# Performance work log

Measured on AMD Instinct MI355X. Metric: run time of the kernel, lower is better.

The kernel has to match this reference:

```python
import jax, jax.numpy as jnp
import numpy as np

H = 4        # attention heads
C = 32       # embedding_size (out_channels per head)
B = 8        # graphs per batch
NPER = 2048  # nodes (Hi-C bins) per graph
N = B * NPER
E = 1048576  # edges (avg degree 64)
IN = 4       # input_embedding_size
ED = 1       # edge_dim
EPS = 1e-5


def setup_inputs() -> dict:
    key = jax.random.key(0)
    ks = jax.random.split(key, 20)
    x = jax.random.normal(ks[0], (N, IN), jnp.float32)
    # edges stay within their graph so the per-graph reshape in
    # process_graph_batch is semantically consistent
    g = jax.random.randint(ks[1], (E,), 0, B)
    src = g * NPER + jax.random.randint(ks[2], (E,), 0, NPER)
    dst = g * NPER + jax.random.randint(ks[3], (E,), 0, NPER)
    edge_index = jnp.stack([src, dst]).astype(jnp.int32)
    edge_attr = jax.random.uniform(ks[4], (E, ED), jnp.float32)
    batch_index = jnp.repeat(jnp.arange(B, dtype=jnp.int32), NPER)

    def lin(k, i, o):
        return jax.random.normal(k, (i, o), jnp.float32) / np.float32(np.sqrt(i))

    HC = H * C
    inp = dict(
        x=x, edge_index=edge_index, edge_attr=edge_attr, batch_index=batch_index,
        Wq=lin(ks[5], IN, HC), bq=jnp.zeros((HC,), jnp.float32),
        Wk=lin(ks[6], IN, HC), bk=jnp.zeros((HC,), jnp.float32),
        Wv=lin(ks[7], IN, HC), bv=jnp.zeros((HC,), jnp.float32),
        We=lin(ks[8], ED, HC), be=jnp.zeros((HC,), jnp.float32),
        Ws=lin(ks[9], IN, HC), bs=jnp.zeros((HC,), jnp.float32),
        Wbeta=lin(ks[10], 3 * HC, 1),
        Wl=lin(ks[11], HC, C), bl=jnp.zeros((C,), jnp.float32),
        gn_w=jnp.ones((C,), jnp.float32),
        gn_b=jnp.zeros((C,), jnp.float32),
        gn_ms=jnp.ones((C,), jnp.float32),
    )
    return inp


def reference(x, edge_index, edge_attr, batch_index,
              Wq, bq, Wk, bk, Wv, bv, We, be, Ws, bs, Wbeta,
              Wl, bl, gn_w, gn_b, gn_ms):
    src, dst = edge_index[0], edge_index[1]
    n = x.shape[0]
    e = src.shape[0]

    # ---- TransformerConv(in=4, out=32, heads=4, edge_dim=1, beta=True) ----
    q = (x @ Wq + bq).reshape(n, H, C)
    k = (x @ Wk + bk).reshape(n, H, C)
    v = (x @ Wv + bv).reshape(n, H, C)
    ee = (edge_attr @ We + be).reshape(e, H, C)

    kj = k[src] + ee               # [E,H,C] key of source + edge embedding
    vj = v[src] + ee               # [E,H,C]
    qi = q[dst]                    # [E,H,C]
    alpha = jnp.sum(qi * kj, axis=-1) / jnp.sqrt(jnp.float32(C))  # [E,H]

    # segment softmax over incoming edges of each destination node
    amax = jax.ops.segment_max(alpha, dst, num_segments=n)        # [N,H]
    amax = jnp.where(jnp.isfinite(amax), amax, 0.0)
    alpha = jnp.exp(alpha - jax.lax.stop_gradient(amax)[dst])
    denom = jax.ops.segment_sum(alpha, dst, num_segments=n)       # [N,H]
    denom = jnp.where(denom > 0, denom, 1.0)
    alpha = alpha / denom[dst]

    out = jax.ops.segment_sum(alpha[..., None] * vj, dst, num_segments=n)
    out = out.reshape(n, H * C)    # concat heads

    # beta skip connection (root_weight + gated residual)
    x_r = x @ Ws + bs              # [N,H*C]
    beta = jax.nn.sigmoid(jnp.concatenate([out, x_r, out - x_r], axis=-1) @ Wbeta)
    out = beta * x_r + (1.0 - beta) * out

    # ---- Linear + relu ----
    h = jax.nn.relu(out @ Wl + bl)  # [N,C]

    # ---- GraphNorm over each graph in the batch ----
    ones = jnp.ones((n, 1), h.dtype)
    cnt = jax.ops.segment_sum(ones, batch_index, num_segments=B)        # [B,1]
    mean = jax.ops.segment_sum(h, batch_index, num_segments=B) / cnt    # [B,C]
    hc = h - gn_ms * mean[batch_index]
    var = jax.ops.segment_sum(hc * hc, batch_index, num_segments=B) / cnt
    h = hc / jnp.sqrt(var[batch_index] + EPS) * gn_w + gn_b

    # ---- process_graph_batch + InnerProductDecoder ----
    Z = h.reshape(B, NPER, C)
    adj = jax.nn.sigmoid(jnp.einsum('bnc,bmc->bnm', Z, Z))
    return adj[:, None, :, :]      # [B,1,NPER,NPER]
```

## Files before the change

### kernel.cpp

```cpp
#include <hip/hip_runtime.h>

#define NGRAPH 8
#define NPER 2048
#define NN 16384
#define EE 1048576
#define BSH 5
#define NB (NN >> BSH)
#define NPB (1 << BSH)
#define SEG 4096
#define CAP 3584
#define SBLK 128
#define EPB (EE/SBLK)
#define XBOUND 8.0f
#define RSQRT_C 0.17677669529663687f

typedef __attribute__((ext_vector_type(8))) short short8v;
typedef __attribute__((ext_vector_type(4))) float f32x4;

__device__ __forceinline__ float sigmoidf_(float v){ return 1.0f/(1.0f + __expf(-v)); }

__device__ __forceinline__ unsigned short f2bf(float v){
  unsigned u = __float_as_uint(v);
  unsigned r = (u + 0x7FFFu + ((u >> 16) & 1u)) >> 16;
  return (unsigned short)r;
}
__device__ __forceinline__ float bf2f(unsigned short h){
  return __uint_as_float(((unsigned)h) << 16);
}

__global__ __launch_bounds__(256) void k_pre(const float* __restrict__ x,
                      const float* __restrict__ Wq, const float* __restrict__ bq,
                      const float* __restrict__ Wk, const float* __restrict__ bk,
                      const float* __restrict__ be, const float* __restrict__ We,
                      unsigned* __restrict__ cursor,
                      float* __restrict__ P){
  if (blockIdx.x < 2){
    const int b = blockIdx.x*256 + threadIdx.x;
    cursor[b] = (unsigned)b * SEG;
  }
  const int tid = blockIdx.x*256 + threadIdx.x;
  const int n = tid >> 2, h = tid & 3;
  const float4 xn = *(const float4*)&x[n*4];
  float a0=0.f,a1=0.f,a2=0.f,a3=0.f,qw=0.f,bb=0.f;
#pragma unroll
  for (int c=0;c<32;c++){
    int hc = h*32 + c;
    float q = bq[hc] + xn.x*Wq[hc] + xn.y*Wq[128+hc] + xn.z*Wq[256+hc] + xn.w*Wq[384+hc];
    a0 += q*Wk[hc];     a1 += q*Wk[128+hc];
    a2 += q*Wk[256+hc]; a3 += q*Wk[384+hc];
    qw += q*We[hc];
    bb += q*(bk[hc] + be[hc]);
  }
  a0*=RSQRT_C; a1*=RSQRT_C; a2*=RSQRT_C; a3*=RSQRT_C; qw*=RSQRT_C; bb*=RSQRT_C;
  float M = bb + fmaxf(qw, 0.f) + XBOUND*(fabsf(a0)+fabsf(a1)+fabsf(a2)+fabsf(a3));
  float* p = P + n*24 + h*6;
  p[0]=a0; p[1]=a1; p[2]=a2; p[3]=a3; p[4]=qw; p[5]=bb - M;
}

__global__ __launch_bounds__(1024) void k_scatter(const int* __restrict__ ei, const float* __restrict__ ea,
                                                  unsigned* __restrict__ cursor, uint2* __restrict__ rec){
  __shared__ unsigned hl[NB];
  __shared__ unsigned bl[NB];
  __shared__ unsigned ol[NB];
  const int t = threadIdx.x;
  if (t < NB){ hl[t] = 0u; ol[t] = 0u; }
  __syncthreads();
  const int base = blockIdx.x * EPB;
  int d[8], s[8]; float a[8];
#pragma unroll
  for (int k=0;k<8;k++){
    const int e = base + k*1024 + t;
    d[k] = ei[EE + e];
    s[k] = ei[e];
    a[k] = ea[e];
    atomicAdd(&hl[d[k] >> BSH], 1u);
  }
  __syncthreads();
  if (t < NB && hl[t]) bl[t] = atomicAdd(&cursor[t], hl[t]);
  __syncthreads();
#pragma unroll
  for (int k=0;k<8;k++){
    const int b = d[k] >> BSH;
    const unsigned pos = bl[b] + atomicAdd(&ol[b], 1u);
    if (pos < (unsigned)(b+1)*SEG)
      rec[pos] = make_uint2((unsigned)s[k] | ((unsigned)(d[k] & (NPB-1)) << 14), __float_as_uint(a[k]));
  }
}

__global__ __launch_bounds__(512) void k_edge(const float4* __restrict__ x4,
    const float* __restrict__ P,
    const unsigned* __restrict__ cursor,
    const uint2* __restrict__ rec,
    const float* __restrict__ Wv, const float* __restrict__ bv,
    const float* __restrict__ We, const float* __restrict__ be,
    const float* __restrict__ Ws, const float* __restrict__ bs,
    const float* __restrict__ Wb,
    const float* __restrict__ Wl, const float* __restrict__ bl,
    float* __restrict__ hout){
  __shared__ uint2 lrec[CAP];
  __shared__ unsigned cnt[NPB], cof[NPB], rbase[NPB];
  __shared__ float lout[8][130];
  const int t = threadIdx.x, bb = blockIdx.x;
  const int lane = t & 63, wid = t >> 6;
  if (t < NPB){ cnt[t] = 0u; cof[t] = 0u; }
  __syncthreads();
  const unsigned beg = (unsigned)bb * SEG;
  const unsigned end = cursor[bb];
  for (unsigned i = beg + t; i < end; i += 512)
    atomicAdd(&cnt[(rec[i].x >> 14) & (NPB-1)], 1u);
  __syncthreads();
  if (t < 64){
    unsigned v = (t < NPB) ? cnt[t] : 0u;
    unsigned s = v;
#pragma unroll
    for (int off=1; off<NPB; off<<=1){
      unsigned o = __shfl_up(s, off, 64);
      if (t >= off) s += o;
    }
    if (t < NPB) rbase[t] = s - v;
  }
  __syncthreads();
  for (unsigned i = beg + t; i < end; i += 512){
    uint2 r = rec[i];
    unsigned nd = (r.x >> 14) & (NPB-1);
    unsigned pos = rbase[nd] + atomicAdd(&cof[nd], 1u);
    if (pos < CAP) lrec[pos] = r;
  }
  __syncthreads();

  const int h  = lane >> 4;
  const int sl = lane & 15;
  for (int j=0; j<4; j++){
    const int nd = wid*4 + j;
    const int n = bb*NPB + nd;
    float pr[6];
#pragma unroll
    for (int i=0;i<6;i++) pr[i] = P[n*24 + h*6 + i];
    const unsigned sbeg = rbase[nd];
    unsigned send = sbeg + cnt[nd];
    if (send > CAP) send = CAP;

    float s0=0.f, s1=0.f, s2=0.f, s3=0.f, s4=0.f, s5=0.f;
    for (unsigned i = sbeg + sl; i < send; i += 16){
      const uint2 r = lrec[i];
      const int src = r.x & 0x3FFF;
      const float at = __uint_as_float(r.y);
      const float4 xs = x4[src];
      float al = pr[5] + at*pr[4] + pr[0]*xs.x + pr[1]*xs.y + pr[2]*xs.z + pr[3]*xs.w;
      float w = __expf(al);
      s0 += w;
      s1 += w*at;
      s2 += w*xs.x;
      s3 += w*xs.y;
      s4 += w*xs.z;
      s5 += w*xs.w;
    }
#pragma unroll
    for (int off=1; off<16; off<<=1){
      s0 += __shfl_xor(s0, off, 64);
      s1 += __shfl_xor(s1, off, 64);
      s2 += __shfl_xor(s2, off, 64);
      s3 += __shfl_xor(s3, off, 64);
      s4 += __shfl_xor(s4, off, 64);
      s5 += __shfl_xor(s5, off, 64);
    }

    const int hc0 = lane*2, hc1 = hc0 + 1;
    float ov0 = 0.f, ov1 = 0.f;
    if (s0 > 0.f){
      const float inv = 1.0f/s0;
      ov0 = (s2*Wv[hc0] + s3*Wv[128+hc0] + s4*Wv[256+hc0] + s5*Wv[384+hc0] + s1*We[hc0])*inv
            + bv[hc0] + be[hc0];
      ov1 = (s2*Wv[hc1] + s3*Wv[128+hc1] + s4*Wv[256+hc1] + s5*Wv[384+hc1] + s1*We[hc1])*inv
            + bv[hc1] + be[hc1];
    }
    const float4 xn = x4[n];
    const float xr0 = bs[hc0] + xn.x*Ws[hc0] + xn.y*Ws[128+hc0] + xn.z*Ws[256+hc0] + xn.w*Ws[384+hc0];
    const float xr1 = bs[hc1] + xn.x*Ws[hc1] + xn.y*Ws[128+hc1] + xn.z*Ws[256+hc1] + xn.w*Ws[384+hc1];

    float part = ov0*Wb[hc0] + xr0*Wb[128+hc0] + (ov0-xr0)*Wb[256+hc0]
               + ov1*Wb[hc1] + xr1*Wb[128+hc1] + (ov1-xr1)*Wb[256+hc1];
#pragma unroll
    for (int off=1; off<64; off<<=1) part += __shfl_xor(part, off, 64);
    const float beta = sigmoidf_(part);
    const float o0 = beta*xr0 + (1.f-beta)*ov0;
    const float o1 = beta*xr1 + (1.f-beta)*ov1;

    lout[wid][hc0] = o0;
    lout[wid][hc1] = o1;

    const int c = lane & 31, half = lane >> 5;
    float acc = 0.f;
#pragma unroll 8
    for (int q2=0; q2<64; q2++){
      int hc = half*64 + q2;
      acc += lout[wid][hc] * Wl[hc*32 + c];
    }
    acc += __shfl_xor(acc, 32, 64);
    if (lane < 32) hout[n*32 + c] = fmaxf(acc + bl[c], 0.f);
  }
}

__global__ __launch_bounds__(1024) void k_statsA(const float* __restrict__ h,
                                                 float* __restrict__ part, float* __restrict__ part2){
  const int blk = blockIdx.x;
  const int t = threadIdx.x; const int c = t & 31, g = t >> 5;
  float s = 0.f, ss = 0.f;
  const int r0 = blk*256 + g;
  for (int r = r0; r < blk*256 + 256; r += 32){
    float v = h[r*32 + c];
    s += v; ss += v*v;
  }
  __shared__ float t1[1024], t2[1024];
  t1[t]=s; t2[t]=ss; __syncthreads();
  for (int off=512; off>=32; off>>=1){
    if (t<off){ t1[t]+=t1[t+off]; t2[t]+=t2[t+off]; }
    __syncthreads();
  }
  if (t<32){ part[blk*32+t] = t1[t]; part2[blk*32+t] = t2[t]; }
}

__global__ __launch_bounds__(1024) void k_norm(const float* __restrict__ h,
                                               const float* __restrict__ part, const float* __restrict__ part2,
                                               const float* __restrict__ gms, const float* __restrict__ gw,
                                               const float* __restrict__ gb,
                                               unsigned short* __restrict__ Zh, unsigned short* __restrict__ Zl){
  const int blk = blockIdx.x; const int b = blk >> 3;
  const int t = threadIdx.x; const int c = t & 31, g = t >> 5;
  float S = 0.f, SS = 0.f;
#pragma unroll
  for (int j=0;j<8;j++){
    S  += part [(b*8+j)*32 + c];
    SS += part2[(b*8+j)*32 + c];
  }
  const float ms = gms[c];
  const float mean = S * (1.0f/NPER);
  const float var = SS*(1.0f/NPER) - mean*mean*ms*(2.0f - ms);
  const float scv = gw[c] * rsqrtf(var + 1e-5f);
  const float mb = ms*mean, ob = gb[c];
  for (int r = blk*256 + g; r < blk*256 + 256; r += 32){
    int idx = r*32 + c;
    float zf = (h[idx] - mb)*scv + ob;
    unsigned short zh = f2bf(zf);
    Zh[idx] = zh;
    Zl[idx] = f2bf(zf - bf2f(zh));
  }
}

__global__ __launch_bounds__(256) void k_gemm(const unsigned short* __restrict__ Zh,
                                              const unsigned short* __restrict__ Zl,
                                              float* __restrict__ out){
  const int lane = threadIdx.x & 63, wid = threadIdx.x >> 6;
  const int z = blockIdx.z;
  const int nr = blockIdx.y*16 + (lane & 15);
  const int tc0 = (blockIdx.x*16 + wid*4) * 16;
  const int ch = (lane >> 4) * 8;
  const size_t zb = (size_t)z * NPER * 32;
  const short8v ah = *(const short8v*)(Zh + zb + (size_t)nr*32 + ch);
  const short8v al = *(const short8v*)(Zl + zb + (size_t)nr*32 + ch);
  const size_t obase = (size_t)z*NPER*NPER + (size_t)(blockIdx.y*16 + (lane>>4)*4)*NPER + (lane & 15);
#pragma unroll
  for (int u=0; u<4; u++){
    const int nc = tc0 + u*16 + (lane & 15);
    const short8v bh = *(const short8v*)(Zh + zb + (size_t)nc*32 + ch);
    const short8v bl = *(const short8v*)(Zl + zb + (size_t)nc*32 + ch);
    f32x4 acc = {0.f, 0.f, 0.f, 0.f};
    acc = __builtin_amdgcn_mfma_f32_16x16x32_bf16(ah, bh, acc, 0, 0, 0);
    acc = __builtin_amdgcn_mfma_f32_16x16x32_bf16(ah, bl, acc, 0, 0, 0);
    acc = __builtin_amdgcn_mfma_f32_16x16x32_bf16(al, bh, acc, 0, 0, 0);
    float* op = out + obase + tc0 + u*16;
#pragma unroll
    for (int jj=0; jj<4; jj++) op[(size_t)jj*NPER] = sigmoidf_(acc[jj]);
  }
}

extern "C" void kernel_launch(void* const* d_in, const int* in_sizes, int n_in,
                              void* d_out, int out_size, void* d_ws, size_t ws_size,
                              hipStream_t stream){
  const float* x  = (const float*)d_in[0];
  const int*   ei = (const int*)d_in[1];
  const float* ea = (const float*)d_in[2];
  const float* Wq = (const float*)d_in[4];
  const float* bq = (const float*)d_in[5];
  const float* Wk = (const float*)d_in[6];
  const float* bk = (const float*)d_in[7];
  const float* Wv = (const float*)d_in[8];
  const float* bv = (const float*)d_in[9];
  const float* We = (const float*)d_in[10];
  const float* be = (const float*)d_in[11];
  const float* Ws = (const float*)d_in[12];
  const float* bs = (const float*)d_in[13];
  const float* Wb = (const float*)d_in[14];
  const float* Wl = (const float*)d_in[15];
  const float* bl = (const float*)d_in[16];
  const float* gw = (const float*)d_in[17];
  const float* gb = (const float*)d_in[18];
  const float* gms= (const float*)d_in[19];
  float* out = (float*)d_out;

  char* p = (char*)d_ws;
  auto bump = [&](size_t bytes)->char*{ char* r = p; p += (bytes + 255) & ~(size_t)255; return r; };
  unsigned* cursor  = (unsigned*)bump((size_t)NB*4);
  float*    P       = (float*)bump((size_t)NN*24*4);
  uint2*    rec     = (uint2*)bump((size_t)NB*SEG*8);
  float*    hbuf    = (float*)bump((size_t)NN*32*4);
  float*    part    = (float*)bump((size_t)64*32*4);
  float*    part2   = (float*)bump((size_t)64*32*4);
  unsigned short* Zh = (unsigned short*)bump((size_t)NN*32*2);
  unsigned short* Zl = (unsigned short*)bump((size_t)NN*32*2);

  hipLaunchKernelGGL(k_pre,  dim3(NN*4/256), dim3(256), 0, stream, x, Wq,bq, Wk,bk, be, We, cursor, P);
  hipLaunchKernelGGL(k_scatter, dim3(SBLK), dim3(1024), 0, stream, ei, ea, cursor, rec);
  hipLaunchKernelGGL(k_edge, dim3(NB), dim3(512), 0, stream,
                     (const float4*)x, P, cursor, rec,
                     Wv, bv, We, be, Ws, bs, Wb, Wl, bl, hbuf);
  hipLaunchKernelGGL(k_statsA, dim3(64), dim3(1024), 0, stream, hbuf, part, part2);
  hipLaunchKernelGGL(k_norm, dim3(64), dim3(1024), 0, stream, hbuf, part, part2, gms, gw, gb, Zh, Zl);
  hipLaunchKernelGGL(k_gemm, dim3(NPER/256, NPER/16, NGRAPH), dim3(256), 0, stream, Zh, Zl, out);
}
```

Measured before the change: 93.22 us.

## Fuse pre, scatter, edge, stats and norm into one cooperative persistent kernel

Combines the five pre-GEMM kernels into a single cooperative kernel of 256 blocks that uses grid syncs between phases, falling back to four separate launches if a cooperative launch fails. Per-graph node features are staged in shared memory so source gathers read LDS instead of global memory, and the record encoding is narrowed to per-graph local indices. GraphNorm partial sums are accumulated inside the edge phase, which removes a separate pass over h. The cost of launches and of the global gather is traded for grid-wide barriers and more LDS per block, with fewer blocks doing two buckets each, and the per-destination record capacity drops from 3584 to 2752.

```diff
diff --git a/kernel.cpp b/kernel.cpp
--- a/kernel.cpp
+++ b/kernel.cpp
@@ -1,16 +1,19 @@
 #include <hip/hip_runtime.h>
+#include <hip/hip_cooperative_groups.h>
+
+namespace cg = cooperative_groups;
 
 #define NGRAPH 8
 #define NPER 2048
 #define NN 16384
 #define EE 1048576
 #define BSH 5
-#define NB (NN >> BSH)
-#define NPB (1 << BSH)
+#define NB 512
+#define NPB 32
 #define SEG 4096
-#define CAP 3584
-#define SBLK 128
-#define EPB (EE/SBLK)
+#define CAP 2752
+#define NBLK 256
+#define EPB (EE/NBLK)
 #define XBOUND 8.0f
 #define RSQRT_C 0.17677669529663687f
 
@@ -21,229 +24,238 @@
 
 __device__ __forceinline__ unsigned short f2bf(float v){
   unsigned u = __float_as_uint(v);
-  unsigned r = (u + 0x7FFFu + ((u >> 16) & 1u)) >> 16;
-  return (unsigned short)r;
+  return (unsigned short)((u + 0x7FFFu + ((u >> 16) & 1u)) >> 16);
 }
 __device__ __forceinline__ float bf2f(unsigned short h){
   return __uint_as_float(((unsigned)h) << 16);
 }
 
-__global__ __launch_bounds__(256) void k_pre(const float* __restrict__ x,
-                      const float* __restrict__ Wq, const float* __restrict__ bq,
-                      const float* __restrict__ Wk, const float* __restrict__ bk,
-                      const float* __restrict__ be, const float* __restrict__ We,
-                      unsigned* __restrict__ cursor,
-                      float* __restrict__ P){
-  if (blockIdx.x < 2){
-    const int b = blockIdx.x*256 + threadIdx.x;
-    cursor[b] = (unsigned)b * SEG;
-  }
-  const int tid = blockIdx.x*256 + threadIdx.x;
-  const int n = tid >> 2, h = tid & 3;
-  const float4 xn = *(const float4*)&x[n*4];
-  float a0=0.f,a1=0.f,a2=0.f,a3=0.f,qw=0.f,bb=0.f;
-#pragma unroll
-  for (int c=0;c<32;c++){
-    int hc = h*32 + c;
-    float q = bq[hc] + xn.x*Wq[hc] + xn.y*Wq[128+hc] + xn.z*Wq[256+hc] + xn.w*Wq[384+hc];
-    a0 += q*Wk[hc];     a1 += q*Wk[128+hc];
-    a2 += q*Wk[256+hc]; a3 += q*Wk[384+hc];
-    qw += q*We[hc];
-    bb += q*(bk[hc] + be[hc]);
-  }
-  a0*=RSQRT_C; a1*=RSQRT_C; a2*=RSQRT_C; a3*=RSQRT_C; qw*=RSQRT_C; bb*=RSQRT_C;
-  float M = bb + fmaxf(qw, 0.f) + XBOUND*(fabsf(a0)+fabsf(a1)+fabsf(a2)+fabsf(a3));
-  float* p = P + n*24 + h*6;
-  p[0]=a0; p[1]=a1; p[2]=a2; p[3]=a3; p[4]=qw; p[5]=bb - M;
-}
-
-__global__ __launch_bounds__(1024) void k_scatter(const int* __restrict__ ei, const float* __restrict__ ea,
-                                                  unsigned* __restrict__ cursor, uint2* __restrict__ rec){
-  __shared__ unsigned hl[NB];
-  __shared__ unsigned bl[NB];
-  __shared__ unsigned ol[NB];
-  const int t = threadIdx.x;
-  if (t < NB){ hl[t] = 0u; ol[t] = 0u; }
-  __syncthreads();
-  const int base = blockIdx.x * EPB;
-  int d[8], s[8]; float a[8];
-#pragma unroll
-  for (int k=0;k<8;k++){
-    const int e = base + k*1024 + t;
-    d[k] = ei[EE + e];
-    s[k] = ei[e];
-    a[k] = ea[e];
-    atomicAdd(&hl[d[k] >> BSH], 1u);
-  }
-  __syncthreads();
-  if (t < NB && hl[t]) bl[t] = atomicAdd(&cursor[t], hl[t]);
-  __syncthreads();
-#pragma unroll
-  for (int k=0;k<8;k++){
-    const int b = d[k] >> BSH;
-    const unsigned pos = bl[b] + atomicAdd(&ol[b], 1u);
-    if (pos < (unsigned)(b+1)*SEG)
-      rec[pos] = make_uint2((unsigned)s[k] | ((unsigned)(d[k] & (NPB-1)) << 14), __float_as_uint(a[k]));
-  }
-}
-
-__global__ __launch_bounds__(512) void k_edge(const float4* __restrict__ x4,
-    const float* __restrict__ P,
-    const unsigned* __restrict__ cursor,
-    const uint2* __restrict__ rec,
-    const float* __restrict__ Wv, const float* __restrict__ bv,
-    const float* __restrict__ We, const float* __restrict__ be,
-    const float* __restrict__ Ws, const float* __restrict__ bs,
-    const float* __restrict__ Wb,
-    const float* __restrict__ Wl, const float* __restrict__ bl,
-    float* __restrict__ hout){
+struct FusedParams {
+  const float4* x4;
+  const int* ei;
+  const float* ea;
+  const float* Wq; const float* bq;
+  const float* Wk; const float* bk;
+  const float* be; const float* We;
+  const float* Wv; const float* bv;
+  const float* Ws; const float* bs;
+  const float* Wb;
+  const float* Wl; const float* bl;
+  const float* gms; const float* gw; const float* gb;
+  unsigned* cursor;
+  float* P;
+  uint2* rec;
+  float* hbuf;
+  float* part; float* part2;
+  unsigned short* Zh; unsigned short* Zl;
+};
+
+__global__ __launch_bounds__(512, 2) void k_fused(FusedParams p, int phases){
+  __shared__ float4 xg[NPER];
   __shared__ uint2 lrec[CAP];
-  __shared__ unsigned cnt[NPB], cof[NPB], rbase[NPB];
-  __shared__ float lout[8][130];
+  __shared__ unsigned cpool[96];
+  __shared__ __align__(16) unsigned char upool[6144];
+
+  unsigned* cnt   = cpool;
+  unsigned* cof   = cpool + 32;
+  unsigned* rbase = cpool + 64;
+  unsigned* shh = (unsigned*)upool;
+  unsigned* shb = (unsigned*)(upool + 2048);
+  unsigned* sho = (unsigned*)(upool + 4096);
+  float (*lout)[128] = (float (*)[128])upool;
+  float* redA = (float*)upool;
+  float* redB = (float*)(upool + 2048);
+
   const int t = threadIdx.x, bb = blockIdx.x;
   const int lane = t & 63, wid = t >> 6;
-  if (t < NPB){ cnt[t] = 0u; cof[t] = 0u; }
-  __syncthreads();
-  const unsigned beg = (unsigned)bb * SEG;
-  const unsigned end = cursor[bb];
-  for (unsigned i = beg + t; i < end; i += 512)
-    atomicAdd(&cnt[(rec[i].x >> 14) & (NPB-1)], 1u);
-  __syncthreads();
-  if (t < 64){
-    unsigned v = (t < NPB) ? cnt[t] : 0u;
-    unsigned s = v;
-#pragma unroll
-    for (int off=1; off<NPB; off<<=1){
-      unsigned o = __shfl_up(s, off, 64);
-      if (t >= off) s += o;
-    }
-    if (t < NPB) rbase[t] = s - v;
-  }
-  __syncthreads();
-  for (unsigned i = beg + t; i < end; i += 512){
-    uint2 r = rec[i];
-    unsigned nd = (r.x >> 14) & (NPB-1);
-    unsigned pos = rbase[nd] + atomicAdd(&cof[nd], 1u);
-    if (pos < CAP) lrec[pos] = r;
-  }
-  __syncthreads();
-
-  const int h  = lane >> 4;
-  const int sl = lane & 15;
-  for (int j=0; j<4; j++){
-    const int nd = wid*4 + j;
-    const int n = bb*NPB + nd;
-    float pr[6];
-#pragma unroll
-    for (int i=0;i<6;i++) pr[i] = P[n*24 + h*6 + i];
-    const unsigned sbeg = rbase[nd];
-    unsigned send = sbeg + cnt[nd];
-    if (send > CAP) send = CAP;
-
-    float s0=0.f, s1=0.f, s2=0.f, s3=0.f, s4=0.f, s5=0.f;
-    for (unsigned i = sbeg + sl; i < send; i += 16){
-      const uint2 r = lrec[i];
-      const int src = r.x & 0x3FFF;
-      const float at = __uint_as_float(r.y);
-      const float4 xs = x4[src];
-      float al = pr[5] + at*pr[4] + pr[0]*xs.x + pr[1]*xs.y + pr[2]*xs.z + pr[3]*xs.w;
-      float w = __expf(al);
-      s0 += w;
-      s1 += w*at;
-      s2 += w*xs.x;
-      s3 += w*xs.y;
-      s4 += w*xs.z;
-      s5 += w*xs.w;
-    }
-#pragma unroll
-    for (int off=1; off<16; off<<=1){
-      s0 += __shfl_xor(s0, off, 64);
-      s1 += __shfl_xor(s1, off, 64);
-      s2 += __shfl_xor(s2, off, 64);
-      s3 += __shfl_xor(s3, off, 64);
-      s4 += __shfl_xor(s4, off, 64);
-      s5 += __shfl_xor(s5, off, 64);
-    }
-
-    const int hc0 = lane*2, hc1 = hc0 + 1;
-    float ov0 = 0.f, ov1 = 0.f;
-    if (s0 > 0.f){
-      const float inv = 1.0f/s0;
-      ov0 = (s2*Wv[hc0] + s3*Wv[128+hc0] + s4*Wv[256+hc0] + s5*Wv[384+hc0] + s1*We[hc0])*inv
-            + bv[hc0] + be[hc0];
-      ov1 = (s2*Wv[hc1] + s3*Wv[128+hc1] + s4*Wv[256+hc1] + s5*Wv[384+hc1] + s1*We[hc1])*inv
-            + bv[hc1] + be[hc1];
-    }
-    const float4 xn = x4[n];
-    const float xr0 = bs[hc0] + xn.x*Ws[hc0] + xn.y*Ws[128+hc0] + xn.z*Ws[256+hc0] + xn.w*Ws[384+hc0];
-    const float xr1 = bs[hc1] + xn.x*Ws[hc1] + xn.y*Ws[128+hc1] + xn.z*Ws[256+hc1] + xn.w*Ws[384+hc1];
-
-    float part = ov0*Wb[hc0] + xr0*Wb[128+hc0] + (ov0-xr0)*Wb[256+hc0]
-               + ov1*Wb[hc1] + xr1*Wb[128+hc1] + (ov1-xr1)*Wb[256+hc1];
-#pragma unroll
-    for (int off=1; off<64; off<<=1) part += __shfl_xor(part, off, 64);
-    const float beta = sigmoidf_(part);
-    const float o0 = beta*xr0 + (1.f-beta)*ov0;
-    const float o1 = beta*xr1 + (1.f-beta)*ov1;
-
-    lout[wid][hc0] = o0;
-    lout[wid][hc1] = o1;
-
-    const int c = lane & 31, half = lane >> 5;
-    float acc = 0.f;
+
+  if (phases & 1){
+    if (bb == 0) p.cursor[t] = (unsigned)t * SEG;
+    if (bb < 128){
+      const int tid = (bb << 9) + t;
+      const int n = tid >> 2, h = tid & 3;
+      const float4 xn = p.x4[n];
+      float a0=0.f,a1=0.f,a2=0.f,a3=0.f,qw=0.f,bc=0.f;
+#pragma unroll
+      for (int c=0;c<32;c++){
+        const int hc = (h<<5) + c;
+        float q = p.bq[hc] + xn.x*p.Wq[hc] + xn.y*p.Wq[128+hc] + xn.z*p.Wq[256+hc] + xn.w*p.Wq[384+hc];
+        a0 += q*p.Wk[hc];     a1 += q*p.Wk[128+hc];
+        a2 += q*p.Wk[256+hc]; a3 += q*p.Wk[384+hc];
+        qw += q*p.We[hc];
+        bc += q*(p.bk[hc] + p.be[hc]);
+      }
+      a0*=RSQRT_C; a1*=RSQRT_C; a2*=RSQRT_C; a3*=RSQRT_C; qw*=RSQRT_C; bc*=RSQRT_C;
+      const float M = bc + fmaxf(qw,0.f) + XBOUND*(fabsf(a0)+fabsf(a1)+fabsf(a2)+fabsf(a3));
+      float* pp = p.P + (size_t)tid*6;
+      pp[0]=a0; pp[1]=a1; pp[2]=a2; pp[3]=a3; pp[4]=qw; pp[5]=bc - M;
+    }
+  }
+  if (phases == 15) cg::this_grid().sync();
+
+  if (phases & 2){
+    shh[t] = 0u; sho[t] = 0u;
+    __syncthreads();
+    const int base = bb * EPB;
+    int dv[8]; uint2 rv[8];
+#pragma unroll
+    for (int k=0;k<8;k++){
+      const int e = base + k*512 + t;
+      const int d = p.ei[EE + e];
+      dv[k] = d >> BSH;
+      rv[k] = make_uint2((unsigned)(p.ei[e] & (NPER-1)) | ((unsigned)(d & (NPB-1)) << 11),
+                         __float_as_uint(p.ea[e]));
+      atomicAdd(&shh[dv[k]], 1u);
+    }
+    __syncthreads();
+    if (shh[t]) shb[t] = atomicAdd(&p.cursor[t], shh[t]);
+    __syncthreads();
+#pragma unroll
+    for (int k=0;k<8;k++){
+      const unsigned pos = shb[dv[k]] + atomicAdd(&sho[dv[k]], 1u);
+      if (pos < (unsigned)(dv[k]+1)*SEG)
+        p.rec[pos] = rv[k];
+    }
+  }
+  if (phases == 15) cg::this_grid().sync();
+
+  if (phases & 4){
+    const int g = bb >> 5;
+    for (int i = t; i < NPER; i += 512) xg[i] = p.x4[g*NPER + i];
+    const int h  = lane >> 4;
+    const int sl = lane & 15;
+    float sS = 0.f, sSS = 0.f;
+
+    for (int bk = 0; bk < 2; bk++){
+      const int bu = bb*2 + bk;
+      __syncthreads();
+      if (t < NPB){ cnt[t] = 0u; cof[t] = 0u; }
+      __syncthreads();
+      const unsigned beg = (unsigned)bu * SEG;
+      const unsigned end = p.cursor[bu];
+      for (unsigned i = beg + t; i < end; i += 512)
+        atomicAdd(&cnt[(p.rec[i].x >> 11) & (NPB-1)], 1u);
+      __syncthreads();
+      if (t < 64){
+        unsigned v = (t < NPB) ? cnt[t] : 0u;
+        unsigned s = v;
+#pragma unroll
+        for (int off=1; off<NPB; off<<=1){
+          unsigned o = __shfl_up(s, off, 64);
+          if (t >= off) s += o;
+        }
+        if (t < NPB) rbase[t] = s - v;
+      }
+      __syncthreads();
+      for (unsigned i = beg + t; i < end; i += 512){
+        uint2 r = p.rec[i];
+        unsigned nd = (r.x >> 11) & (NPB-1);
+        unsigned pos = rbase[nd] + atomicAdd(&cof[nd], 1u);
+        if (pos < CAP) lrec[pos] = r;
+      }
+      __syncthreads();
+
+      for (int j=0; j<4; j++){
+        const int nd = wid*4 + j;
+        const int n = bu*NPB + nd;
+        float pr[6];
+#pragma unroll
+        for (int i=0;i<6;i++) pr[i] = p.P[(size_t)n*24 + h*6 + i];
+        const unsigned sbeg = rbase[nd];
+        unsigned send = sbeg + cnt[nd];
+        if (send > CAP) send = CAP;
+
+        float s0=0.f, s1=0.f, s2=0.f, s3=0.f, s4=0.f, s5=0.f;
+        for (unsigned i = sbeg + sl; i < send; i += 16){
+          const uint2 r = lrec[i];
+          const float4 xs = xg[r.x & (NPER-1)];
+          const float at = __uint_as_float(r.y);
+          float al = pr[5] + at*pr[4] + pr[0]*xs.x + pr[1]*xs.y + pr[2]*xs.z + pr[3]*xs.w;
+          float w = __expf(al);
+          s0 += w;  s1 += w*at;
+          s2 += w*xs.x; s3 += w*xs.y; s4 += w*xs.z; s5 += w*xs.w;
+        }
+#pragma unroll
+        for (int off=1; off<16; off<<=1){
+          s0 += __shfl_xor(s0, off, 64);
+          s1 += __shfl_xor(s1, off, 64);
+          s2 += __shfl_xor(s2, off, 64);
+          s3 += __shfl_xor(s3, off, 64);
+          s4 += __shfl_xor(s4, off, 64);
+          s5 += __shfl_xor(s5, off, 64);
+        }
+
+        const int hc0 = lane*2, hc1 = hc0 + 1;
+        float ov0 = 0.f, ov1 = 0.f;
+        if (s0 > 0.f){
+          const float inv = 1.0f/s0;
+          ov0 = (s2*p.Wv[hc0] + s3*p.Wv[128+hc0] + s4*p.Wv[256+hc0] + s5*p.Wv[384+hc0] + s1*p.We[hc0])*inv
+                + p.bv[hc0] + p.be[hc0];
+          ov1 = (s2*p.Wv[hc1] + s3*p.Wv[128+hc1] + s4*p.Wv[256+hc1] + s5*p.Wv[384+hc1] + s1*p.We[hc1])*inv
+                + p.bv[hc1] + p.be[hc1];
+        }
+        const float4 xn = xg[n & (NPER-1)];
+        const float xr0 = p.bs[hc0] + xn.x*p.Ws[hc0] + xn.y*p.Ws[128+hc0] + xn.z*p.Ws[256+hc0] + xn.w*p.Ws[384+hc0];
+        const float xr1 = p.bs[hc1] + xn.x*p.Ws[hc1] + xn.y*p.Ws[128+hc1] + xn.z*p.Ws[256+hc1] + xn.w*p.Ws[384+hc1];
+
+        float part = ov0*p.Wb[hc0] + xr0*p.Wb[128+hc0] + (ov0-xr0)*p.Wb[256+hc0]
+                   + ov1*p.Wb[hc1] + xr1*p.Wb[128+hc1] + (ov1-xr1)*p.Wb[256+hc1];
+#pragma unroll
+        for (int off=1; off<64; off<<=1) part += __shfl_xor(part, off, 64);
+        const float beta = sigmoidf_(part);
+        const float o0 = beta*xr0 + (1.f-beta)*ov0;
+        const float o1 = beta*xr1 + (1.f-beta)*ov1;
+
+        lout[wid][hc0] = o0;
+        lout[wid][hc1] = o1;
+
+        const int c = lane & 31, half = lane >> 5;
+        float acc = 0.f;
 #pragma unroll 8
-    for (int q2=0; q2<64; q2++){
-      int hc = half*64 + q2;
-      acc += lout[wid][hc] * Wl[hc*32 + c];
-    }
-    acc += __shfl_xor(acc, 32, 64);
-    if (lane < 32) hout[n*32 + c] = fmaxf(acc + bl[c], 0.f);
-  }
-}
-
-__global__ __launch_bounds__(1024) void k_statsA(const float* __restrict__ h,
-                                                 float* __restrict__ part, float* __restrict__ part2){
-  const int blk = blockIdx.x;
-  const int t = threadIdx.x; const int c = t & 31, g = t >> 5;
-  float s = 0.f, ss = 0.f;
-  const int r0 = blk*256 + g;
-  for (int r = r0; r < blk*256 + 256; r += 32){
-    float v = h[r*32 + c];
-    s += v; ss += v*v;
-  }
-  __shared__ float t1[1024], t2[1024];
-  t1[t]=s; t2[t]=ss; __syncthreads();
-  for (int off=512; off>=32; off>>=1){
-    if (t<off){ t1[t]+=t1[t+off]; t2[t]+=t2[t+off]; }
-    __syncthreads();
-  }
-  if (t<32){ part[blk*32+t] = t1[t]; part2[blk*32+t] = t2[t]; }
-}
-
-__global__ __launch_bounds__(1024) void k_norm(const float* __restrict__ h,
-                                               const float* __restrict__ part, const float* __restrict__ part2,
-                                               const float* __restrict__ gms, const float* __restrict__ gw,
-                                               const float* __restrict__ gb,
-                                               unsigned short* __restrict__ Zh, unsigned short* __restrict__ Zl){
-  const int blk = blockIdx.x; const int b = blk >> 3;
-  const int t = threadIdx.x; const int c = t & 31, g = t >> 5;
-  float S = 0.f, SS = 0.f;
-#pragma unroll
-  for (int j=0;j<8;j++){
-    S  += part [(b*8+j)*32 + c];
-    SS += part2[(b*8+j)*32 + c];
-  }
-  const float ms = gms[c];
-  const float mean = S * (1.0f/NPER);
-  const float var = SS*(1.0f/NPER) - mean*mean*ms*(2.0f - ms);
-  const float scv = gw[c] * rsqrtf(var + 1e-5f);
-  const float mb = ms*mean, ob = gb[c];
-  for (int r = blk*256 + g; r < blk*256 + 256; r += 32){
-    int idx = r*32 + c;
-    float zf = (h[idx] - mb)*scv + ob;
-    unsigned short zh = f2bf(zf);
-    Zh[idx] = zh;
-    Zl[idx] = f2bf(zf - bf2f(zh));
+        for (int q2=0; q2<64; q2++){
+          int hc = half*64 + q2;
+          acc += lout[wid][hc] * p.Wl[hc*32 + c];
+        }
+        acc += __shfl_xor(acc, 32, 64);
+        if (lane < 32){
+          const float hv = fmaxf(acc + p.bl[c], 0.f);
+          p.hbuf[(size_t)n*32 + c] = hv;
+          sS += hv; sSS += hv*hv;
+        }
+      }
+    }
+    __syncthreads();
+    redA[t] = (lane < 32) ? sS  : 0.f;
+    redB[t] = (lane < 32) ? sSS : 0.f;
+    __syncthreads();
+    for (int off=256; off>=32; off>>=1){
+      if (t < off){ redA[t] += redA[t+off]; redB[t] += redB[t+off]; }
+      __syncthreads();
+    }
+    if (t < 32){ p.part[bb*32 + t] = redA[t]; p.part2[bb*32 + t] = redB[t]; }
+  }
+  if (phases == 15) cg::this_grid().sync();
+
+  if (phases & 8){
+    const int g = bb >> 5;
+    const int c = t & 31;
+    float S = 0.f, SS = 0.f;
+    for (int j=0; j<32; j++){
+      S  += p.part [((size_t)g*32 + j)*32 + c];
+      SS += p.part2[((size_t)g*32 + j)*32 + c];
+    }
+    const float ms = p.gms[c];
+    const float mean = S * (1.0f/NPER);
+    const float var = SS*(1.0f/NPER) - mean*mean*ms*(2.0f - ms);
+    const float scv = p.gw[c] * rsqrtf(var + 1e-5f);
+    const float mb = ms*mean, ob = p.gb[c];
+    for (int rr = t>>5; rr < 64; rr += 16){
+      const size_t idx = ((size_t)bb*64 + rr)*32 + c;
+      const float zf = (p.hbuf[idx] - mb)*scv + ob;
+      const unsigned short zh = f2bf(zf);
+      p.Zh[idx] = zh;
+      p.Zl[idx] = f2bf(zf - bf2f(zh));
+    }
   }
 }
 
@@ -304,17 +316,28 @@
   float*    P       = (float*)bump((size_t)NN*24*4);
   uint2*    rec     = (uint2*)bump((size_t)NB*SEG*8);
   float*    hbuf    = (float*)bump((size_t)NN*32*4);
-  float*    part    = (float*)bump((size_t)64*32*4);
-  float*    part2   = (float*)bump((size_t)64*32*4);
+  float*    part    = (float*)bump((size_t)NBLK*32*4);
+  float*    part2   = (float*)bump((size_t)NBLK*32*4);
   unsigned short* Zh = (unsigned short*)bump((size_t)NN*32*2);
   unsigned short* Zl = (unsigned short*)bump((size_t)NN*32*2);
 
-  hipLaunchKernelGGL(k_pre,  dim3(NN*4/256), dim3(256), 0, stream, x, Wq,bq, Wk,bk, be, We, cursor, P);
-  hipLaunchKernelGGL(k_scatter, dim3(SBLK), dim3(1024), 0, stream, ei, ea, cursor, rec);
-  hipLaunchKernelGGL(k_edge, dim3(NB), dim3(512), 0, stream,
-                     (const float4*)x, P, cursor, rec,
-                     Wv, bv, We, be, Ws, bs, Wb, Wl, bl, hbuf);
-  hipLaunchKernelGGL(k_statsA, dim3(64), dim3(1024), 0, stream, hbuf, part, part2);
-  hipLaunchKernelGGL(k_norm, dim3(64), dim3(1024), 0, stream, hbuf, part, part2, gms, gw, gb, Zh, Zl);
+  FusedParams fp;
+  fp.x4 = (const float4*)x; fp.ei = ei; fp.ea = ea;
+  fp.Wq = Wq; fp.bq = bq; fp.Wk = Wk; fp.bk = bk; fp.be = be; fp.We = We;
+  fp.Wv = Wv; fp.bv = bv; fp.Ws = Ws; fp.bs = bs; fp.Wb = Wb;
+  fp.Wl = Wl; fp.bl = bl; fp.gms = gms; fp.gw = gw; fp.gb = gb;
+  fp.cursor = cursor; fp.P = P; fp.rec = rec; fp.hbuf = hbuf;
+  fp.part = part; fp.part2 = part2; fp.Zh = Zh; fp.Zl = Zl;
+
+  int ph_all = 15;
+  void* kargs[] = { (void*)&fp, (void*)&ph_all };
+  hipError_t err = hipLaunchCooperativeKernel((const void*)k_fused, dim3(NBLK), dim3(512),
+                                              kargs, 0, stream);
+  if (err != hipSuccess){
+    hipLaunchKernelGGL(k_fused, dim3(NBLK), dim3(512), 0, stream, fp, 1);
+    hipLaunchKernelGGL(k_fused, dim3(NBLK), dim3(512), 0, stream, fp, 2);
+    hipLaunchKernelGGL(k_fused, dim3(NBLK), dim3(512), 0, stream, fp, 4);
+    hipLaunchKernelGGL(k_fused, dim3(NBLK), dim3(512), 0, stream, fp, 8);
+  }
   hipLaunchKernelGGL(k_gemm, dim3(NPER/256, NPER/16, NGRAPH), dim3(256), 0, stream, Zh, Zl, out);
 }
```

Result: slower. 205.0 us (+119.9%).
